# Kernel optimization log

Measured on AMD Instinct MI355X. Metric: run time of the kernel, lower is better.

## Reference

```python
import jax, jax.numpy as jnp
import numpy as np

N_NODES = 100000
N_EDGES = 640000
D_IN = 128
EPS = 1e-12  # torch F.normalize eps


def _sage_conv(x, src, dst, Wl, Wr, b):
    # mean aggregation of neighbor features: for each dst node, mean of x[src]
    n = x.shape[0]
    agg = jax.ops.segment_sum(x[src], dst, num_segments=n)
    cnt = jax.ops.segment_sum(jnp.ones((src.shape[0],), x.dtype), dst, num_segments=n)
    agg = agg / jnp.maximum(cnt, 1.0)[:, None]
    # out = lin_l(agg) + lin_r(x); PyG puts bias in lin_l
    h = agg @ Wl.T + b + x @ Wr.T
    # normalize=True -> L2 normalize rows
    norm = jnp.linalg.norm(h, axis=-1, keepdims=True)
    return h / jnp.maximum(norm, EPS)


def setup_inputs() -> dict:
    key = jax.random.key(0)
    ks = jax.random.split(key, 12)
    hid = 256
    inp = {
        "x": jax.random.normal(ks[0], (N_NODES, D_IN), dtype=jnp.float32),
        "edge_index": jax.random.randint(ks[1], (2, N_EDGES), 0, N_NODES, dtype=jnp.int64),
        "W1l": jax.random.normal(ks[2], (hid, D_IN), dtype=jnp.float32) * 0.05,
        "W1r": jax.random.normal(ks[3], (hid, D_IN), dtype=jnp.float32) * 0.05,
        "b1": jax.random.normal(ks[4], (hid,), dtype=jnp.float32) * 0.05,
        "W2l": jax.random.normal(ks[5], (hid // 2, hid), dtype=jnp.float32) * 0.05,
        "W2r": jax.random.normal(ks[6], (hid // 2, hid), dtype=jnp.float32) * 0.05,
        "b2": jax.random.normal(ks[7], (hid // 2,), dtype=jnp.float32) * 0.05,
        "W3l": jax.random.normal(ks[8], (2, hid // 2), dtype=jnp.float32) * 0.05,
        "W3r": jax.random.normal(ks[9], (2, hid // 2), dtype=jnp.float32) * 0.05,
        "b3": jax.random.normal(ks[10], (2,), dtype=jnp.float32) * 0.05,
    }
    return inp


def reference(x, edge_index, W1l, W1r, b1, W2l, W2r, b2, W3l, W3r, b3):
    src, dst = edge_index[0], edge_index[1]
    h = _sage_conv(x, src, dst, W1l, W1r, b1)
    h = jax.nn.relu(h)  # dropout is identity in eval mode
    h = _sage_conv(h, src, dst, W2l, W2r, b2)
    h = jax.nn.relu(h)
    h = _sage_conv(h, src, dst, W3l, W3r, b3)
    return jax.nn.log_softmax(h, axis=1)
```

## Files before the change

### kernel.cpp

```cpp
#include <hip/hip_runtime.h>
#include <math.h>

#define NN 100000
#define NE 640000
#define NBLK 98
#define GBLK 1563

typedef __bf16 bf16_t;
typedef bf16_t bf16x8 __attribute__((ext_vector_type(8)));
typedef float  f32x4  __attribute__((ext_vector_type(4)));


__global__ __launch_bounds__(256) void k_hist(const int* __restrict__ dst,
                                              int* __restrict__ deg) {
    int e = blockIdx.x * 256 + threadIdx.x;
    if (e < NE) atomicAdd(&deg[dst[e]], 1);
}

__global__ __launch_bounds__(1024) void k_bsum(const int* __restrict__ deg,
                                               int* __restrict__ bsum) {
    __shared__ int warr[16];
    int t = threadIdx.x;
    int i = blockIdx.x * 1024 + t;
    int v = (i < NN) ? deg[i] : 0;
    int lane = t & 63, wid = t >> 6;
    #pragma unroll
    for (int off = 32; off > 0; off >>= 1) v += __shfl_xor(v, off, 64);
    if (lane == 0) warr[wid] = v;
    __syncthreads();
    if (t < 16) {
        int s = warr[t];
        #pragma unroll
        for (int off = 8; off > 0; off >>= 1) s += __shfl_xor(s, off, 64);
        if (t == 0) bsum[blockIdx.x] = s;
    }
}

__global__ __launch_bounds__(64) void k_bscan(const int* __restrict__ bsum,
        int* __restrict__ boff, int* __restrict__ rowptr) {
    int lane = threadIdx.x;
    int carry = 0;
    for (int base = 0; base < NBLK; base += 64) {
        int i = base + lane;
        int v = (i < NBLK) ? bsum[i] : 0;
        int s = v;
        #pragma unroll
        for (int off = 1; off < 64; off <<= 1) {
            int u = __shfl_up(s, off, 64);
            if (lane >= off) s += u;
        }
        if (i < NBLK) boff[i] = carry + s - v;
        carry += __shfl(s, 63, 64);
    }
    if (lane == 0) rowptr[NN] = NE;
}

__global__ __launch_bounds__(1024) void k_scan2(const int* __restrict__ deg,
        const int* __restrict__ boff, int* __restrict__ rowptr,
        int* __restrict__ cursor) {
    __shared__ int wsum[16];
    __shared__ int woff[16];
    int t = threadIdx.x;
    int lane = t & 63, wid = t >> 6;
    int i = blockIdx.x * 1024 + t;
    int v = (i < NN) ? deg[i] : 0;
    int s = v;
    #pragma unroll
    for (int off = 1; off < 64; off <<= 1) {
        int u = __shfl_up(s, off, 64);
        if (lane >= off) s += u;
    }
    if (lane == 63) wsum[wid] = s;
    __syncthreads();
    if (wid == 0) {
        int ws = (lane < 16) ? wsum[lane] : 0;
        #pragma unroll
        for (int off = 1; off < 16; off <<= 1) {
            int u = __shfl_up(ws, off, 64);
            if (lane >= off) ws += u;
        }
        if (lane < 16) woff[lane] = ws;
    }
    __syncthreads();
    if (i < NN) {
        int excl = boff[blockIdx.x] + (s - v) + (wid ? woff[wid - 1] : 0);
        rowptr[i] = excl;
        cursor[i] = excl;
    }
}

__global__ __launch_bounds__(256) void k_fill(const int* __restrict__ src,
        const int* __restrict__ dst, int* __restrict__ cursor,
        int* __restrict__ csr) {
    int e = blockIdx.x * 256 + threadIdx.x;
    if (e >= NE) return;
    int p = atomicAdd(&cursor[dst[e]], 1);
    csr[p] = src[e];
}


__global__ __launch_bounds__(256) void k_split_w(const float* __restrict__ W1l,
        const float* __restrict__ W1r, const float* __restrict__ W2l,
        const float* __restrict__ W2r, bf16_t* __restrict__ W1fh,
        bf16_t* __restrict__ W1fl, bf16_t* __restrict__ W2fh,
        bf16_t* __restrict__ W2fl) {
    int b = blockIdx.x, t = threadIdx.x;
    float f;
    bf16_t* Wfh;
    bf16_t* Wfl;
    int j;
    if (b < 256) {
        j = b;
        f = (t < 128) ? W1l[j * 128 + t] : W1r[j * 128 + (t - 128)];
        Wfh = W1fh; Wfl = W1fl;
    } else {
        j = b - 256;
        f = (j < 128) ? W2l[j * 256 + t] : W2r[(j - 128) * 256 + t];
        Wfh = W2fh; Wfl = W2fl;
    }
    bf16_t h = (bf16_t)f;
    bf16_t l = (bf16_t)(f - (float)h);
    int idx = (((j >> 4) * 8 + (t >> 5)) * 64 + ((t >> 3) & 3) * 16 + (j & 15)) * 8 + (t & 7);
    Wfh[idx] = h;
    Wfl[idx] = l;
}


__device__ __forceinline__ void splitv(float4 v0, float4 v1,
                                       bf16x8& h, bf16x8& l) {
    float f[8] = {v0.x, v0.y, v0.z, v0.w, v1.x, v1.y, v1.z, v1.w};
    #pragma unroll
    for (int i = 0; i < 8; i++) {
        bf16_t hi = (bf16_t)f[i];
        h[i] = hi;
        l[i] = (bf16_t)(f[i] - (float)hi);
    }
}

__global__ __launch_bounds__(256, 2) void k_gemm_fused(const float* __restrict__ Ax,
        const int* __restrict__ rowptr, const int* __restrict__ csr,
        const bf16_t* __restrict__ W1fh, const bf16_t* __restrict__ W1fl,
        const bf16_t* __restrict__ W2fh, const bf16_t* __restrict__ W2fl,
        const float* __restrict__ bias,
        float* __restrict__ C2a, float* __restrict__ C2r) {
    __shared__ bf16_t sHf[64 * 256], sLf[64 * 256];
    __shared__ float pr[64][4];
    int t = threadIdx.x;
    int wave = t >> 6, lane = t & 63, quad = lane >> 4, l16 = lane & 15;
    int r0 = blockIdx.x * 64;
    int arow = t >> 2, aseg = t & 3;
    int grow = r0 + arow; if (grow >= NN) grow = NN - 1;
    {
        int beg = rowptr[grow], end = rowptr[grow + 1];
        float iv = 1.0f / (float)max(end - beg, 1);
        f32x4 ac[8] = {};
        for (int e = beg; e < end; e++) {
            int s = csr[e];
            const float* prow = &Ax[(size_t)s * 128 + aseg * 8];
            #pragma unroll
            for (int it = 0; it < 4; it++) {
                ac[it * 2]     += *(const f32x4*)(prow + it * 32);
                ac[it * 2 + 1] += *(const f32x4*)(prow + it * 32 + 4);
            }
        }
        #pragma unroll
        for (int it = 0; it < 4; it++) {
            f32x4 v0 = ac[it * 2] * iv;
            f32x4 v1 = ac[it * 2 + 1] * iv;
            bf16x8 h8, l8;
            #pragma unroll
            for (int i = 0; i < 4; i++) {
                bf16_t hh = (bf16_t)v0[i];
                h8[i] = hh; l8[i] = (bf16_t)(v0[i] - (float)hh);
            }
            #pragma unroll
            for (int i = 0; i < 4; i++) {
                bf16_t hh = (bf16_t)v1[i];
                h8[i + 4] = hh; l8[i + 4] = (bf16_t)(v1[i] - (float)hh);
            }
            int idx = (((arow >> 4) * 8 + it) * 64 + aseg * 16 + (arow & 15)) * 8;
            *(bf16x8*)&sHf[idx] = h8;
            *(bf16x8*)&sLf[idx] = l8;
        }
    }
    #pragma unroll
    for (int it = 4; it < 8; it++) {
        const float* p = &Ax[(size_t)grow * 128 + (it - 4) * 32 + aseg * 8];
        bf16x8 h8, l8;
        splitv(*(const float4*)p, *(const float4*)(p + 4), h8, l8);
        int idx = (((arow >> 4) * 8 + it) * 64 + aseg * 16 + (arow & 15)) * 8;
        *(bf16x8*)&sHf[idx] = h8;
        *(bf16x8*)&sLf[idx] = l8;
    }
    __syncthreads();
    f32x4 acc[4][4] = {};
    for (int it = 0; it < 8; it++) {
        bf16x8 bh[4], bl[4];
        #pragma unroll
        for (int nt = 0; nt < 4; nt++) {
            size_t fo = (size_t)(((wave * 4 + nt) * 8 + it) * 64 + lane) * 8;
            bh[nt] = *(const bf16x8*)&W1fh[fo];
            bl[nt] = *(const bf16x8*)&W1fl[fo];
        }
        #pragma unroll
        for (int mt = 0; mt < 4; mt++) {
            int fb = ((mt * 8 + it) * 64 + lane) * 8;
            bf16x8 ah = *(bf16x8*)&sHf[fb];
            bf16x8 al = *(bf16x8*)&sLf[fb];
            #pragma unroll
            for (int nt = 0; nt < 4; nt++) {
                acc[mt][nt] = __builtin_amdgcn_mfma_f32_16x16x32_bf16(ah, bh[nt], acc[mt][nt], 0, 0, 0);
                acc[mt][nt] = __builtin_amdgcn_mfma_f32_16x16x32_bf16(al, bh[nt], acc[mt][nt], 0, 0, 0);
                acc[mt][nt] = __builtin_amdgcn_mfma_f32_16x16x32_bf16(ah, bl[nt], acc[mt][nt], 0, 0, 0);
            }
        }
    }
    float bcol[4];
    #pragma unroll
    for (int nt = 0; nt < 4; nt++) bcol[nt] = bias[wave * 64 + nt * 16 + l16];
    #pragma unroll
    for (int mt = 0; mt < 4; mt++)
        #pragma unroll
        for (int nt = 0; nt < 4; nt++)
            #pragma unroll
            for (int rg = 0; rg < 4; rg++)
                acc[mt][nt][rg] += bcol[nt];
    float ss[4][4];
    #pragma unroll
    for (int mt = 0; mt < 4; mt++)
        #pragma unroll
        for (int rg = 0; rg < 4; rg++) {
            float s = 0.f;
            #pragma unroll
            for (int nt = 0; nt < 4; nt++) s += acc[mt][nt][rg] * acc[mt][nt][rg];
            #pragma unroll
            for (int off = 1; off < 16; off <<= 1) s += __shfl_xor(s, off, 64);
            ss[mt][rg] = s;
        }
    if (l16 == 0) {
        #pragma unroll
        for (int mt = 0; mt < 4; mt++)
            #pragma unroll
            for (int rg = 0; rg < 4; rg++)
                pr[mt * 16 + quad * 4 + rg][wave] = ss[mt][rg];
    }
    __syncthreads();
    #pragma unroll
    for (int mt = 0; mt < 4; mt++)
        #pragma unroll
        for (int rg = 0; rg < 4; rg++) {
            int r = mt * 16 + quad * 4 + rg;
            float tot = pr[r][0] + pr[r][1] + pr[r][2] + pr[r][3];
            float inv = 1.0f / fmaxf(sqrtf(tot), 1e-12f);
            #pragma unroll
            for (int nt = 0; nt < 4; nt++) {
                int c = wave * 64 + nt * 16 + l16;
                float v = fmaxf(acc[mt][nt][rg] * inv, 0.f);
                bf16_t h = (bf16_t)v;
                bf16_t l = (bf16_t)(v - (float)h);
                int idx = (((r >> 4) * 8 + (c >> 5)) * 64 + ((c >> 3) & 3) * 16 + (r & 15)) * 8 + (c & 7);
                sHf[idx] = h;
                sLf[idx] = l;
            }
        }
    __syncthreads();
    f32x4 acc2[4][4] = {};
    for (int it = 0; it < 8; it++) {
        bf16x8 bh[4], bl[4];
        #pragma unroll
        for (int nt = 0; nt < 4; nt++) {
            size_t fo = (size_t)(((wave * 4 + nt) * 8 + it) * 64 + lane) * 8;
            bh[nt] = *(const bf16x8*)&W2fh[fo];
            bl[nt] = *(const bf16x8*)&W2fl[fo];
        }
        #pragma unroll
        for (int mt = 0; mt < 4; mt++) {
            int fb = ((mt * 8 + it) * 64 + lane) * 8;
            bf16x8 ah = *(bf16x8*)&sHf[fb];
            bf16x8 al = *(bf16x8*)&sLf[fb];
            #pragma unroll
            for (int nt = 0; nt < 4; nt++) {
                acc2[mt][nt] = __builtin_amdgcn_mfma_f32_16x16x32_bf16(ah, bh[nt], acc2[mt][nt], 0, 0, 0);
                acc2[mt][nt] = __builtin_amdgcn_mfma_f32_16x16x32_bf16(al, bh[nt], acc2[mt][nt], 0, 0, 0);
                acc2[mt][nt] = __builtin_amdgcn_mfma_f32_16x16x32_bf16(ah, bl[nt], acc2[mt][nt], 0, 0, 0);
            }
        }
    }
    float* dstb = (wave < 2) ? C2a : C2r;
    int cb = (wave < 2) ? (wave * 64) : ((wave - 2) * 64);
    #pragma unroll
    for (int mt = 0; mt < 4; mt++)
        #pragma unroll
        for (int rg = 0; rg < 4; rg++) {
            int row = r0 + mt * 16 + quad * 4 + rg;
            if (row >= NN) continue;
            #pragma unroll
            for (int nt = 0; nt < 4; nt++) {
                int col = cb + nt * 16 + l16;
                dstb[(size_t)row * 128 + col] = acc2[mt][nt][rg];
            }
        }
}


__global__ __launch_bounds__(256) void k_gather_combine(const float* __restrict__ C2a,
        const float* __restrict__ C2r,
        const int* __restrict__ rowptr, const int* __restrict__ csr,
        const float* __restrict__ b2, const float* __restrict__ W3l,
        float* __restrict__ h2, float* __restrict__ q3) {
    __shared__ float sw[256];
    int t = threadIdx.x;
    sw[t] = W3l[t];
    __syncthreads();
    int tid = blockIdx.x * 256 + t;
    int node = tid >> 5;
    if (node >= NN) return;
    int l = tid & 31;
    int lane4 = l << 2;
    int beg = rowptr[node], end = rowptr[node + 1];
    float4 acc = make_float4(0.f, 0.f, 0.f, 0.f);
    int e = beg;
    for (; e + 1 < end; e += 2) {
        int s0 = csr[e], s1 = csr[e + 1];
        float4 v0 = *(const float4*)(C2a + (size_t)s0 * 128 + lane4);
        float4 v1 = *(const float4*)(C2a + (size_t)s1 * 128 + lane4);
        acc.x += v0.x + v1.x; acc.y += v0.y + v1.y;
        acc.z += v0.z + v1.z; acc.w += v0.w + v1.w;
    }
    if (e < end) {
        int s0 = csr[e];
        float4 v0 = *(const float4*)(C2a + (size_t)s0 * 128 + lane4);
        acc.x += v0.x; acc.y += v0.y; acc.z += v0.z; acc.w += v0.w;
    }
    float iv = 1.0f / (float)max(end - beg, 1);
    float4 r = *(const float4*)&C2r[(size_t)node * 128 + lane4];
    float4 b = *(const float4*)&b2[lane4];
    float v0 = acc.x * iv + r.x + b.x;
    float v1 = acc.y * iv + r.y + b.y;
    float v2 = acc.z * iv + r.z + b.z;
    float v3 = acc.w * iv + r.w + b.w;
    float s = v0 * v0 + v1 * v1 + v2 * v2 + v3 * v3;
    #pragma unroll
    for (int off = 16; off > 0; off >>= 1) s += __shfl_xor(s, off, 64);
    float invn = 1.0f / fmaxf(sqrtf(s), 1e-12f);
    float4 o;
    o.x = fmaxf(v0 * invn, 0.f); o.y = fmaxf(v1 * invn, 0.f);
    o.z = fmaxf(v2 * invn, 0.f); o.w = fmaxf(v3 * invn, 0.f);
    *(float4*)&h2[(size_t)node * 128 + lane4] = o;
    float a0 = o.x * sw[lane4] + o.y * sw[lane4+1] + o.z * sw[lane4+2] + o.w * sw[lane4+3];
    float a1 = o.x * sw[128+lane4] + o.y * sw[129+lane4] + o.z * sw[130+lane4] + o.w * sw[131+lane4];
    #pragma unroll
    for (int off = 16; off > 0; off >>= 1) {
        a0 += __shfl_xor(a0, off, 64);
        a1 += __shfl_xor(a1, off, 64);
    }
    if (l == 0) {
        q3[2 * node] = a0;
        q3[2 * node + 1] = a1;
    }
}


__global__ __launch_bounds__(256) void k_final(const float* __restrict__ h2,
        const float* __restrict__ W3r, const float* __restrict__ b3,
        const float* __restrict__ q3, const int* __restrict__ rowptr,
        const int* __restrict__ csr, float* __restrict__ out) {
    __shared__ float sw[256];
    int t = threadIdx.x;
    sw[t] = W3r[t];
    __syncthreads();
    int i = blockIdx.x * 256 + t;
    if (i >= NN) return;
    int beg = rowptr[i], end = rowptr[i + 1];
    float g0 = 0.f, g1 = 0.f;
    for (int e = beg; e < end; e++) {
        int s = csr[e];
        g0 += q3[2 * s];
        g1 += q3[2 * s + 1];
    }
    float ivd = 1.0f / (float)max(end - beg, 1);
    g0 *= ivd; g1 *= ivd;
    const float4* row = (const float4*)(h2 + (size_t)i * 128);
    float a0 = 0.f, a1 = 0.f;
    #pragma unroll
    for (int q = 0; q < 32; q++) {
        float4 v = row[q];
        a0 += v.x * sw[4*q] + v.y * sw[4*q+1] + v.z * sw[4*q+2] + v.w * sw[4*q+3];
        a1 += v.x * sw[128+4*q] + v.y * sw[129+4*q] + v.z * sw[130+4*q] + v.w * sw[131+4*q];
    }
    float v0 = g0 + a0 + b3[0];
    float v1 = g1 + a1 + b3[1];
    float invn = 1.0f / fmaxf(sqrtf(v0 * v0 + v1 * v1), 1e-12f);
    v0 *= invn; v1 *= invn;
    float mx = fmaxf(v0, v1);
    float l = logf(expf(v0 - mx) + expf(v1 - mx));
    out[2 * i] = v0 - mx - l;
    out[2 * i + 1] = v1 - mx - l;
}


extern "C" void kernel_launch(void* const* d_in, const int* in_sizes, int n_in,
                              void* d_out, int out_size, void* d_ws, size_t ws_size,
                              hipStream_t stream) {
    const float* x   = (const float*)d_in[0];
    const int*   ei  = (const int*)d_in[1];
    const float* W1l = (const float*)d_in[2];
    const float* W1r = (const float*)d_in[3];
    const float* b1  = (const float*)d_in[4];
    const float* W2l = (const float*)d_in[5];
    const float* W2r = (const float*)d_in[6];
    const float* b2  = (const float*)d_in[7];
    const float* W3l = (const float*)d_in[8];
    const float* W3r = (const float*)d_in[9];
    const float* b3  = (const float*)d_in[10];
    float* out = (float*)d_out;
    const int* src = ei;
    const int* dst = ei + NE;

    int* deg    = (int*)d_ws;
    int* rowptr = deg + 102400;
    int* cursor = rowptr + 102400;
    int* csr    = cursor + 102400;
    int* bsum   = csr + 655360;
    int* boff   = bsum + 128;
    bf16_t* W1h  = (bf16_t*)(boff + 128);
    bf16_t* W1lo = W1h + 65536;
    bf16_t* W2h  = W1lo + 65536;
    bf16_t* W2lo = W2h + 65536;
    float* C2a  = (float*)(W2lo + 65536);
    float* C2r  = C2a + (size_t)GBLK * 64 * 128;
    float* h2   = C2r + (size_t)GBLK * 64 * 128;
    float* q3   = h2 + 12800000;

    hipMemsetAsync(deg, 0, NN * sizeof(int), stream);
    k_hist<<<(NE + 255) / 256, 256, 0, stream>>>(dst, deg);
    k_bsum<<<NBLK, 1024, 0, stream>>>(deg, bsum);
    k_bscan<<<1, 64, 0, stream>>>(bsum, boff, rowptr);
    k_scan2<<<NBLK, 1024, 0, stream>>>(deg, boff, rowptr, cursor);
    k_fill<<<(NE + 255) / 256, 256, 0, stream>>>(src, dst, cursor, csr);

    k_split_w<<<512, 256, 0, stream>>>(W1l, W1r, W2l, W2r, W1h, W1lo, W2h, W2lo);

    k_gemm_fused<<<GBLK, 256, 0, stream>>>(x, rowptr, csr, W1h, W1lo, W2h, W2lo, b1, C2a, C2r);

    k_gather_combine<<<(NN * 32 + 255) / 256, 256, 0, stream>>>(C2a, C2r, rowptr, csr, b2, W3l, h2, q3);

    k_final<<<(NN + 255) / 256, 256, 0, stream>>>(h2, W3r, b3, q3, rowptr, csr, out);
}
```

Measured before the change: 379.5 us.

## Halve fused GEMM row tile to 32 and rework neighbor gather mapping

Shrinks the fused two-layer GEMM block from 64 to 32 rows, which halves LDS and accumulator registers and raises the launch-bounds occupancy hint from 2 to 4 blocks per CU, doubling the grid. The neighbor mean gather now uses all 256 threads, 8 per node with 16 contiguous columns each, and unrolls edges by two for more memory-level parallelism. The self-feature split now uses only half the threads. Because 100000 divides evenly by 32, bounds checks are dropped. The trade-off is that W1 and W2 fragments are reloaded from global memory twice as often per row.

```diff
diff --git a/kernel.cpp b/kernel.cpp
--- a/kernel.cpp
+++ b/kernel.cpp
@@ -4,7 +4,7 @@
 #define NN 100000
 #define NE 640000
 #define NBLK 98
-#define GBLK 1563
+#define GBLK 3125
 
 typedef __bf16 bf16_t;
 typedef bf16_t bf16x8 __attribute__((ext_vector_type(8)));
@@ -137,63 +137,82 @@
     }
 }
 
-__global__ __launch_bounds__(256, 2) void k_gemm_fused(const float* __restrict__ Ax,
+__device__ __forceinline__ void split2(f32x4 a, f32x4 b,
+                                       bf16x8& h, bf16x8& l) {
+    #pragma unroll
+    for (int i = 0; i < 4; i++) {
+        bf16_t hi = (bf16_t)a[i];
+        h[i] = hi; l[i] = (bf16_t)(a[i] - (float)hi);
+    }
+    #pragma unroll
+    for (int i = 0; i < 4; i++) {
+        bf16_t hi = (bf16_t)b[i];
+        h[i + 4] = hi; l[i + 4] = (bf16_t)(b[i] - (float)hi);
+    }
+}
+
+__global__ __launch_bounds__(256, 4) void k_gemm_fused(const float* __restrict__ Ax,
         const int* __restrict__ rowptr, const int* __restrict__ csr,
         const bf16_t* __restrict__ W1fh, const bf16_t* __restrict__ W1fl,
         const bf16_t* __restrict__ W2fh, const bf16_t* __restrict__ W2fl,
         const float* __restrict__ bias,
         float* __restrict__ C2a, float* __restrict__ C2r) {
-    __shared__ bf16_t sHf[64 * 256], sLf[64 * 256];
-    __shared__ float pr[64][4];
+    __shared__ bf16_t sHf[32 * 256], sLf[32 * 256];
+    __shared__ float pr[32][4];
     int t = threadIdx.x;
     int wave = t >> 6, lane = t & 63, quad = lane >> 4, l16 = lane & 15;
-    int r0 = blockIdx.x * 64;
-    int arow = t >> 2, aseg = t & 3;
-    int grow = r0 + arow; if (grow >= NN) grow = NN - 1;
-    {
-        int beg = rowptr[grow], end = rowptr[grow + 1];
-        float iv = 1.0f / (float)max(end - beg, 1);
-        f32x4 ac[8] = {};
-        for (int e = beg; e < end; e++) {
-            int s = csr[e];
-            const float* prow = &Ax[(size_t)s * 128 + aseg * 8];
-            #pragma unroll
-            for (int it = 0; it < 4; it++) {
-                ac[it * 2]     += *(const f32x4*)(prow + it * 32);
-                ac[it * 2 + 1] += *(const f32x4*)(prow + it * 32 + 4);
-            }
-        }
-        #pragma unroll
-        for (int it = 0; it < 4; it++) {
-            f32x4 v0 = ac[it * 2] * iv;
-            f32x4 v1 = ac[it * 2 + 1] * iv;
+    int r0 = blockIdx.x * 32;
+    if (t < 128) {
+        int arow = t >> 2, aseg = t & 3;
+        int grow = r0 + arow;
+        #pragma unroll
+        for (int it = 4; it < 8; it++) {
+            const float* p = &Ax[(size_t)grow * 128 + (it - 4) * 32 + aseg * 8];
             bf16x8 h8, l8;
-            #pragma unroll
-            for (int i = 0; i < 4; i++) {
-                bf16_t hh = (bf16_t)v0[i];
-                h8[i] = hh; l8[i] = (bf16_t)(v0[i] - (float)hh);
-            }
-            #pragma unroll
-            for (int i = 0; i < 4; i++) {
-                bf16_t hh = (bf16_t)v1[i];
-                h8[i + 4] = hh; l8[i + 4] = (bf16_t)(v1[i] - (float)hh);
-            }
+            splitv(*(const float4*)p, *(const float4*)(p + 4), h8, l8);
             int idx = (((arow >> 4) * 8 + it) * 64 + aseg * 16 + (arow & 15)) * 8;
             *(bf16x8*)&sHf[idx] = h8;
             *(bf16x8*)&sLf[idx] = l8;
         }
     }
-    #pragma unroll
-    for (int it = 4; it < 8; it++) {
-        const float* p = &Ax[(size_t)grow * 128 + (it - 4) * 32 + aseg * 8];
+    {
+        int node = t >> 3, seg = t & 7;
+        int gn = r0 + node;
+        int beg = rowptr[gn], end = rowptr[gn + 1];
+        int c0 = seg << 4;
+        f32x4 a0 = {}, a1 = {}, a2 = {}, a3 = {};
+        int e = beg;
+        for (; e + 1 < end; e += 2) {
+            int s0 = csr[e], s1 = csr[e + 1];
+            const float* p0 = Ax + (size_t)s0 * 128 + c0;
+            const float* p1 = Ax + (size_t)s1 * 128 + c0;
+            a0 += *(const f32x4*)(p0);      a0 += *(const f32x4*)(p1);
+            a1 += *(const f32x4*)(p0 + 4);  a1 += *(const f32x4*)(p1 + 4);
+            a2 += *(const f32x4*)(p0 + 8);  a2 += *(const f32x4*)(p1 + 8);
+            a3 += *(const f32x4*)(p0 + 12); a3 += *(const f32x4*)(p1 + 12);
+        }
+        if (e < end) {
+            const float* p0 = Ax + (size_t)csr[e] * 128 + c0;
+            a0 += *(const f32x4*)(p0);
+            a1 += *(const f32x4*)(p0 + 4);
+            a2 += *(const f32x4*)(p0 + 8);
+            a3 += *(const f32x4*)(p0 + 12);
+        }
+        float iv = 1.0f / (float)max(end - beg, 1);
+        a0 *= iv; a1 *= iv; a2 *= iv; a3 *= iv;
+        int it = seg >> 1, half = seg & 1;
         bf16x8 h8, l8;
-        splitv(*(const float4*)p, *(const float4*)(p + 4), h8, l8);
-        int idx = (((arow >> 4) * 8 + it) * 64 + aseg * 16 + (arow & 15)) * 8;
+        split2(a0, a1, h8, l8);
+        int idx = (((node >> 4) * 8 + it) * 64 + (half * 2 + 0) * 16 + (node & 15)) * 8;
         *(bf16x8*)&sHf[idx] = h8;
         *(bf16x8*)&sLf[idx] = l8;
-    }
-    __syncthreads();
-    f32x4 acc[4][4] = {};
+        split2(a2, a3, h8, l8);
+        idx = (((node >> 4) * 8 + it) * 64 + (half * 2 + 1) * 16 + (node & 15)) * 8;
+        *(bf16x8*)&sHf[idx] = h8;
+        *(bf16x8*)&sLf[idx] = l8;
+    }
+    __syncthreads();
+    f32x4 acc[2][4] = {};
     for (int it = 0; it < 8; it++) {
         bf16x8 bh[4], bl[4];
         #pragma unroll
@@ -203,7 +222,7 @@
             bl[nt] = *(const bf16x8*)&W1fl[fo];
         }
         #pragma unroll
-        for (int mt = 0; mt < 4; mt++) {
+        for (int mt = 0; mt < 2; mt++) {
             int fb = ((mt * 8 + it) * 64 + lane) * 8;
             bf16x8 ah = *(bf16x8*)&sHf[fb];
             bf16x8 al = *(bf16x8*)&sLf[fb];
@@ -219,15 +238,15 @@
     #pragma unroll
     for (int nt = 0; nt < 4; nt++) bcol[nt] = bias[wave * 64 + nt * 16 + l16];
     #pragma unroll
-    for (int mt = 0; mt < 4; mt++)
+    for (int mt = 0; mt < 2; mt++)
         #pragma unroll
         for (int nt = 0; nt < 4; nt++)
             #pragma unroll
             for (int rg = 0; rg < 4; rg++)
                 acc[mt][nt][rg] += bcol[nt];
-    float ss[4][4];
-    #pragma unroll
-    for (int mt = 0; mt < 4; mt++)
+    float ss[2][4];
+    #pragma unroll
+    for (int mt = 0; mt < 2; mt++)
         #pragma unroll
         for (int rg = 0; rg < 4; rg++) {
             float s = 0.f;
@@ -239,14 +258,14 @@
         }
     if (l16 == 0) {
         #pragma unroll
-        for (int mt = 0; mt < 4; mt++)
+        for (int mt = 0; mt < 2; mt++)
             #pragma unroll
             for (int rg = 0; rg < 4; rg++)
                 pr[mt * 16 + quad * 4 + rg][wave] = ss[mt][rg];
     }
     __syncthreads();
     #pragma unroll
-    for (int mt = 0; mt < 4; mt++)
+    for (int mt = 0; mt < 2; mt++)
         #pragma unroll
         for (int rg = 0; rg < 4; rg++) {
             int r = mt * 16 + quad * 4 + rg;
@@ -264,7 +283,7 @@
             }
         }
     __syncthreads();
-    f32x4 acc2[4][4] = {};
+    f32x4 acc2[2][4] = {};
     for (int it = 0; it < 8; it++) {
         bf16x8 bh[4], bl[4];
         #pragma unroll
@@ -274,7 +293,7 @@
             bl[nt] = *(const bf16x8*)&W2fl[fo];
         }
         #pragma unroll
-        for (int mt = 0; mt < 4; mt++) {
+        for (int mt = 0; mt < 2; mt++) {
             int fb = ((mt * 8 + it) * 64 + lane) * 8;
             bf16x8 ah = *(bf16x8*)&sHf[fb];
             bf16x8 al = *(bf16x8*)&sLf[fb];
@@ -289,11 +308,10 @@
     float* dstb = (wave < 2) ? C2a : C2r;
     int cb = (wave < 2) ? (wave * 64) : ((wave - 2) * 64);
     #pragma unroll
-    for (int mt = 0; mt < 4; mt++)
+    for (int mt = 0; mt < 2; mt++)
         #pragma unroll
         for (int rg = 0; rg < 4; rg++) {
             int row = r0 + mt * 16 + quad * 4 + rg;
-            if (row >= NN) continue;
             #pragma unroll
             for (int nt = 0; nt < 4; nt++) {
                 int col = cb + nt * 16 + l16;
@@ -428,8 +446,8 @@
     bf16_t* W2h  = W1lo + 65536;
     bf16_t* W2lo = W2h + 65536;
     float* C2a  = (float*)(W2lo + 65536);
-    float* C2r  = C2a + (size_t)GBLK * 64 * 128;
-    float* h2   = C2r + (size_t)GBLK * 64 * 128;
+    float* C2r  = C2a + (size_t)NN * 128;
+    float* h2   = C2r + (size_t)NN * 128;
     float* q3   = h2 + 12800000;
 
     hipMemsetAsync(deg, 0, NN * sizeof(int), stream);
```

Result: faster. 361.0 us (-4.9%).
